# Kernel tuning notes

Measured on AMD Instinct MI355X. Metric: run time of the kernel, lower is better.

Reference implementation:

```python
import jax, jax.numpy as jnp
import numpy as np

NQ = 4  # n_qubits
NL = 2  # n_qlayers


def _rx(state, theta, wire):
    # state: (B, 2,...,2) complex; theta: (B,) RX rotation angles
    c = jnp.cos(theta * 0.5)[:, None]
    s = jnp.sin(theta * 0.5)[:, None]
    st = jnp.moveaxis(state, wire + 1, 1)
    sh = st.shape
    st = st.reshape(sh[0], 2, -1)
    a0, a1 = st[:, 0], st[:, 1]
    n0 = c * a0 - 1j * s * a1
    n1 = -1j * s * a0 + c * a1
    st = jnp.stack([n0, n1], axis=1).reshape(sh)
    return jnp.moveaxis(st, 1, wire + 1)


def _cnot(state, ctrl, tgt):
    st = jnp.moveaxis(state, (ctrl + 1, tgt + 1), (1, 2))
    st = jnp.stack([st[:, 0], st[:, 1, ::-1]], axis=1)
    return jnp.moveaxis(st, (1, 2), (ctrl + 1, tgt + 1))


def _vqc(y, W):
    # AngleEmbedding (RX) + BasicEntanglerLayers (RX + CNOT ring), PauliZ expvals.
    # y: (B, NQ) angles; W: (NL, NQ); returns (B, NQ)
    B = y.shape[0]
    state = jnp.zeros((B,) + (2,) * NQ, jnp.complex64)
    state = state.at[(slice(None),) + (0,) * NQ].set(1.0)
    for w in range(NQ):
        state = _rx(state, y[:, w], w)
    for l in range(W.shape[0]):
        for w in range(NQ):
            state = _rx(state, jnp.broadcast_to(W[l, w], (B,)), w)
        for w in range(NQ):
            state = _cnot(state, w, (w + 1) % NQ)
    probs = state.real ** 2 + state.imag ** 2  # (B, 2,2,2,2)
    z = jnp.array([1.0, -1.0], probs.dtype)
    exps = []
    for w in range(NQ):
        sign = z.reshape((1,) + (1,) * w + (2,) + (1,) * (NQ - 1 - w))
        exps.append(jnp.sum(probs * sign, axis=tuple(range(1, NQ + 1))))
    return jnp.stack(exps, axis=1)


def setup_inputs() -> dict:
    key = jax.random.key(0)
    ks = jax.random.split(key, 12)
    B, T, F, H = 1024, 64, 32, 8
    two_pi = 2.0 * np.pi
    return {
        "x": jax.random.normal(ks[0], (B, T, F), jnp.float32),
        "w_in": jax.random.normal(ks[1], (NQ, F + H), jnp.float32) * 0.1,
        "b_in": jnp.zeros((NQ,), jnp.float32),
        "w_out": jax.random.normal(ks[2], (H, NQ), jnp.float32) * 0.1,
        "b_out": jnp.zeros((H,), jnp.float32),
        "wq_f": jax.random.uniform(ks[3], (NL, NQ), jnp.float32, 0.0, two_pi),
        "wq_i": jax.random.uniform(ks[4], (NL, NQ), jnp.float32, 0.0, two_pi),
        "wq_u": jax.random.uniform(ks[5], (NL, NQ), jnp.float32, 0.0, two_pi),
        "wq_o": jax.random.uniform(ks[6], (NL, NQ), jnp.float32, 0.0, two_pi),
        "w_fc": jax.random.normal(ks[7], (1, H), jnp.float32) * 0.1,
        "b_fc": jnp.zeros((1,), jnp.float32),
    }


def reference(x, w_in, b_in, w_out, b_out, wq_f, wq_i, wq_u, wq_o, w_fc, b_fc):
    B, T, F = x.shape
    H = w_out.shape[0]
    h0 = jnp.zeros((B, H), x.dtype)
    c0 = jnp.zeros((B, H), x.dtype)

    def step(carry, x_t):
        h, c = carry
        v = jnp.concatenate([h, x_t], axis=1)           # (B, H+F)
        y = v @ w_in.T + b_in                           # (B, NQ)
        gate = lambda Wq: _vqc(y, Wq) @ w_out.T + b_out  # (B, H)
        f = jax.nn.sigmoid(gate(wq_f))
        i = jax.nn.sigmoid(gate(wq_i))
        g = jnp.tanh(gate(wq_u))
        o = jax.nn.sigmoid(gate(wq_o))
        c = f * c + i * g
        h = o * jnp.tanh(c)
        return (h, c), None

    (h, c), _ = jax.lax.scan(step, (h0, c0), jnp.swapaxes(x, 0, 1))
    return h @ w_fc.T + b_fc  # (B, 1)
```

## Files before the change

### kernel.cpp

```cpp
#include <hip/hip_runtime.h>
#include <math.h>


#define NQ 4
#define NL 2
#define BB 1024
#define TT 64
#define FF 32
#define HH 8

typedef float v2f __attribute__((ext_vector_type(2)));
typedef unsigned uv2 __attribute__((ext_vector_type(2)));
#define FMA2(a, b, c) __builtin_elementwise_fma((a), (b), (c))

#define RX_W(wv, cc, ss) do {                                   \
    const int str_ = 8 >> (wv);                                 \
    _Pragma("unroll")                                           \
    for (int lo_ = 0; lo_ < 16; ++lo_) {                        \
      if ((lo_ & str_) == 0) {                                  \
        const int hi_ = lo_ | str_;                             \
        float a0r = ar[lo_], a0i = ai[lo_];                     \
        float a1r = ar[hi_], a1i = ai[hi_];                     \
        ar[lo_] = fmaf((cc), a0r,  (ss)*a1i);                   \
        ai[lo_] = fmaf((cc), a0i, -(ss)*a1r);                   \
        ar[hi_] = fmaf((cc), a1r,  (ss)*a0i);                   \
        ai[hi_] = fmaf((cc), a1i, -(ss)*a0r);                   \
      }                                                         \
    }                                                           \
} while (0)

#define CNOT_W(cw, tw) do {                                     \
    const int cb_ = 1 << (3-(cw));                              \
    const int tb_ = 1 << (3-(tw));                              \
    _Pragma("unroll")                                           \
    for (int ix_ = 0; ix_ < 16; ++ix_) {                        \
      if ((ix_ & cb_) && !(ix_ & tb_)) {                        \
        const int jx_ = ix_ | tb_;                              \
        float tr_ = ar[ix_]; ar[ix_] = ar[jx_]; ar[jx_] = tr_;  \
        float ti_ = ai[ix_]; ai[ix_] = ai[jx_]; ai[jx_] = ti_;  \
      }                                                         \
    }                                                           \
} while (0)

#define QUAD_BCAST(x, CTRL) \
    __int_as_float(__builtin_amdgcn_mov_dpp(__float_as_int(x), (CTRL), 0xf, 0xf, true))
#define ROW_ROR(x, N) \
    __int_as_float(__builtin_amdgcn_mov_dpp(__float_as_int(x), 0x120 + (N), 0xf, 0xf, true))
#define SWZ_X16(x) \
    __int_as_float(__builtin_amdgcn_ds_swizzle(__float_as_int(x), 0x401F))

#if __has_builtin(__builtin_amdgcn_permlane16_swap)
__device__ __forceinline__ float permx16(float s, int lane) {
    uv2 r = __builtin_amdgcn_permlane16_swap(__builtin_bit_cast(unsigned, s),
                                             __builtin_bit_cast(unsigned, s),
                                             false, false);
    unsigned pick = (lane & 16) ? r.x : r.y;
    return __builtin_bit_cast(float, pick);
}
#else
__device__ __forceinline__ float permx16(float s, int lane) {
    (void)lane;
    return SWZ_X16(s);
}
#endif

#define TPASS(ST) do {                                                       \
    for (int i_ = threadIdx.x; i_ < 432; i_ += 64) {                         \
      int gw_ = i_ / 27; int r_ = i_ - gw_*27;                               \
      int hi_ = r_ / (ST); int lo_ = r_ - hi_*(ST);                          \
      float* row_ = sC + gw_*84; int p0_ = hi_*3*(ST) + lo_;                 \
      float f0_ = row_[p0_], f1_ = row_[p0_+(ST)], f2_ = row_[p0_+2*(ST)];   \
      row_[p0_]          = (f0_ + f1_ + f2_) * 0.3333333333333333f;          \
      row_[p0_+(ST)]     = (2.0f*f0_ - f1_ - f2_) * 0.3333333333333333f;     \
      row_[p0_+2*(ST)]   = (f1_ - f2_) * 0.5773502691896258f;                \
    }                                                                        \
    __syncthreads();                                                         \
} while (0)

#define C3V(k) ((k) == 26 ? c3t : (((k) & 1) ? cp[(k) >> 1].y : cp[(k) >> 1].x))

__global__ __launch_bounds__(64, 1)
void qlstm32p_kernel(const float* __restrict__ x,
                     const float* __restrict__ w_in,
                     const float* __restrict__ b_in,
                     const float* __restrict__ w_out,
                     const float* __restrict__ b_out,
                     const float* __restrict__ wq_f,
                     const float* __restrict__ wq_i,
                     const float* __restrict__ wq_u,
                     const float* __restrict__ wq_o,
                     const float* __restrict__ w_fc,
                     const float* __restrict__ b_fc,
                     float* __restrict__ out) {
    __shared__ float sC[16 * 84];
    __shared__ __align__(16) float sXW[2 * 65 * 4];

    const int lane = threadIdx.x;
    const int w    = lane & 3;
    const int j    = (lane >> 2) & 7;
    const int e    = lane >> 5;

    {
        const float b0 = b_in[0], b1 = b_in[1], b2 = b_in[2], b3 = b_in[3];
        #pragma unroll
        for (int r = 0; r < 8; ++r) {
            int slot = lane + 64 * r;
            int ee = slot >> 8;
            int tt = (slot >> 2) & 63;
            int ww = slot & 3;
            const float* xr = x + ((size_t)(blockIdx.x * 2 + ee) * TT + tt) * FF;
            float bb = (ww == 0) ? b0 : (ww == 1) ? b1 : (ww == 2) ? b2 : b3;
            const float* wrow = w_in + ww * 40 + 8;
            float acc = bb;
            #pragma unroll
            for (int k = 0; k < 8; ++k) {
                float4 xv = *reinterpret_cast<const float4*>(xr + 4 * k);
                acc = fmaf(xv.x, wrow[4*k+0],
                      fmaf(xv.y, wrow[4*k+1],
                      fmaf(xv.z, wrow[4*k+2],
                      fmaf(xv.w, wrow[4*k+3], acc))));
            }
            sXW[(ee * 65 + tt) * 4 + ww] = acc;
        }
    }

    for (int sidx = lane; sidx < 324; sidx += 64) {
        int g = sidx / 81;
        int p = sidx - g * 81;
        int t0 = p / 27; int rem = p - t0 * 27;
        int t1 = rem / 9; rem -= t1 * 9;
        int t2 = rem / 3; int t3 = rem - t2 * 3;

        const float s3h = 0.8660254037844386f;
        float c0 = (t0 == 0) ? 1.0f : 0.5f;
        float s0 = (t0 == 0) ? 0.0f : ((t0 == 1) ? s3h : -s3h);
        float c1 = (t1 == 0) ? 1.0f : 0.5f;
        float s1 = (t1 == 0) ? 0.0f : ((t1 == 1) ? s3h : -s3h);
        float c2 = (t2 == 0) ? 1.0f : 0.5f;
        float s2 = (t2 == 0) ? 0.0f : ((t2 == 1) ? s3h : -s3h);
        float c3v = (t3 == 0) ? 1.0f : 0.5f;
        float s3v = (t3 == 0) ? 0.0f : ((t3 == 1) ? s3h : -s3h);

        const float* wq = (g == 0) ? wq_f : (g == 1) ? wq_i : (g == 2) ? wq_u : wq_o;
        float lc[NL * NQ], ls[NL * NQ];
        #pragma unroll
        for (int a = 0; a < NL * NQ; ++a) {
            float ang = wq[a] * 0.5f;
            lc[a] = __cosf(ang);
            ls[a] = __sinf(ang);
        }

        float m01[4], m23[4];
        m01[0] = c0 * c1;  m01[1] = c0 * s1;  m01[2] = s0 * c1;  m01[3] = s0 * s1;
        m23[0] = c2 * c3v; m23[1] = c2 * s3v; m23[2] = s2 * c3v; m23[3] = s2 * s3v;
        float ar[16], ai[16];
        #pragma unroll
        for (int b0 = 0; b0 < 2; ++b0)
        #pragma unroll
        for (int b1 = 0; b1 < 2; ++b1)
        #pragma unroll
        for (int b2 = 0; b2 < 2; ++b2)
        #pragma unroll
        for (int b3 = 0; b3 < 2; ++b3) {
            const int idx = (b0 << 3) | (b1 << 2) | (b2 << 1) | b3;
            const int pc  = (b0 + b1 + b2 + b3) & 3;
            float m = m01[(b0 << 1) | b1] * m23[(b2 << 1) | b3];
            float re, im;
            if (pc == 0)      { re =  m;   im = 0.0f; }
            else if (pc == 1) { re = 0.0f; im = -m;   }
            else if (pc == 2) { re = -m;   im = 0.0f; }
            else              { re = 0.0f; im =  m;   }
            ar[idx] = re; ai[idx] = im;
        }

        #pragma unroll
        for (int l = 0; l < NL; ++l) {
            RX_W(0, lc[l*4+0], ls[l*4+0]);
            RX_W(1, lc[l*4+1], ls[l*4+1]);
            RX_W(2, lc[l*4+2], ls[l*4+2]);
            RX_W(3, lc[l*4+3], ls[l*4+3]);
            CNOT_W(0, 1); CNOT_W(1, 2); CNOT_W(2, 3); CNOT_W(3, 0);
        }

        float e0 = 0.f, e1 = 0.f, e2 = 0.f, e3 = 0.f;
        #pragma unroll
        for (int idx = 0; idx < 16; ++idx) {
            float pv = fmaf(ar[idx], ar[idx], ai[idx] * ai[idx]);
            e0 += (idx & 8) ? -pv : pv;
            e1 += (idx & 4) ? -pv : pv;
            e2 += (idx & 2) ? -pv : pv;
            e3 += (idx & 1) ? -pv : pv;
        }
        sC[(g * 4 + 0) * 84 + p] = e0;
        sC[(g * 4 + 1) * 84 + p] = e1;
        sC[(g * 4 + 2) * 84 + p] = e2;
        sC[(g * 4 + 3) * 84 + p] = e3;
    }
    __syncthreads();

    TPASS(27); TPASS(9); TPASS(3); TPASS(1);

    v2f E0[13], E1[13], E2[13];
    float e0s, e1s, e2s;
    {
        const float x0 = w_out[j * 4 + 0], x1 = w_out[j * 4 + 1];
        const float x2 = w_out[j * 4 + 2], x3 = w_out[j * 4 + 3];
        const float bo = b_out[j];
        const float* r0 = sC + (w * 4 + 0) * 84;
        const float* r1 = sC + (w * 4 + 1) * 84;
        const float* r2 = sC + (w * 4 + 2) * 84;
        const float* r3 = sC + (w * 4 + 3) * 84;
        #define DVAL(i) (fmaf(x0, r0[(i)], fmaf(x1, r1[(i)], fmaf(x2, r2[(i)], x3 * r3[(i)]))) \
                         + (((i) == 0) ? bo : 0.0f))
        #pragma unroll
        for (int p = 0; p < 13; ++p) {
            E0[p] = v2f{DVAL(6*p + 0), DVAL(6*p + 3)};
            E1[p] = v2f{DVAL(6*p + 1), DVAL(6*p + 4)};
            E2[p] = v2f{DVAL(6*p + 2), DVAL(6*p + 5)};
        }
        e0s = DVAL(78); e1s = DVAL(79); e2s = DVAL(80);
        #undef DVAL
    }
    #pragma unroll
    for (int i = 0; i < 13; ++i)
        asm volatile("" : "+v"(E0[i]), "+v"(E1[i]), "+v"(E2[i]));
    asm volatile("" : "+v"(e0s), "+v"(e1s), "+v"(e2s));

    const float wh  = w_in[w * 40 + j];
    const float wfc = w_fc[j];

    const bool  isG  = (w == 2);
    const float inS  = isG ? 2.0f : 1.0f;
    const float outS = isG ? 2.0f : 1.0f;
    const float outB = isG ? -1.0f : 0.0f;

    const float* sxw = sXW + e * 260 + w;

    float cc = 0.0f, hh = 0.0f;
    float xwv = sxw[0];

    for (int t = 0; t < TT; ++t) {
        float xwn = sxw[4 * (t + 1)];

        float p = hh * wh;
        float s = p + ROW_ROR(p, 4);
        s = s + ROW_ROR(s, 8);
        const float y = xwv + s + permx16(s, lane);

        const float u = __cosf(y), v = __sinf(y);
        const float u0 = QUAD_BCAST(u, 0x00), u1 = QUAD_BCAST(u, 0x55);
        const float u2 = QUAD_BCAST(u, 0xAA), u3 = QUAD_BCAST(u, 0xFF);
        const float v0 = QUAD_BCAST(v, 0x00), v1 = QUAD_BCAST(v, 0x55);
        const float v2 = QUAD_BCAST(v, 0xAA), v3 = QUAD_BCAST(v, 0xFF);

        const v2f u3p = {u3, u3}, v3p = {v3, v3};
        v2f cp[14];
        #pragma unroll
        for (int i = 0; i < 13; ++i)
            cp[i] = FMA2(u3p, E1[i], FMA2(v3p, E2[i], E0[i]));
        const float c3t = fmaf(u3, e1s, fmaf(v3, e2s, e0s));
        float c2v[9];
        #pragma unroll
        for (int i = 0; i < 9; ++i)
            c2v[i] = fmaf(u2, C3V(3*i + 1), fmaf(v2, C3V(3*i + 2), C3V(3*i)));
        const float c1a = fmaf(u1, c2v[1], fmaf(v1, c2v[2], c2v[0]));
        const float c1b = fmaf(u1, c2v[4], fmaf(v1, c2v[5], c2v[3]));
        const float c1c = fmaf(u1, c2v[7], fmaf(v1, c2v[8], c2v[6]));
        const float a = fmaf(u0, c1b, fmaf(v0, c1c, c1a));

        const float sg  = __builtin_amdgcn_rcpf(1.0f + __expf(-inS * a));
        const float act = fmaf(sg, outS, outB);

        const float fv = QUAD_BCAST(act, 0x00), iv = QUAD_BCAST(act, 0x55);
        const float gv = QUAD_BCAST(act, 0xAA), ov = QUAD_BCAST(act, 0xFF);

        cc = fmaf(fv, cc, iv * gv);
        const float th = fmaf(2.0f, __builtin_amdgcn_rcpf(1.0f + __expf(-2.0f * cc)), -1.0f);
        hh = ov * th;

        xwv = xwn;
    }

    float pf = hh * wfc;
    float sf = pf + ROW_ROR(pf, 4);
    sf = sf + ROW_ROR(sf, 8);
    sf = sf + permx16(sf, lane);
    if ((lane & 31) == 0) out[blockIdx.x * 2 + e] = sf + b_fc[0];
}

extern "C" void kernel_launch(void* const* d_in, const int* in_sizes, int n_in,
                              void* d_out, int out_size, void* d_ws, size_t ws_size,
                              hipStream_t stream) {
    const float* x     = (const float*)d_in[0];
    const float* w_in  = (const float*)d_in[1];
    const float* b_in  = (const float*)d_in[2];
    const float* w_out = (const float*)d_in[3];
    const float* b_out = (const float*)d_in[4];
    const float* wq_f  = (const float*)d_in[5];
    const float* wq_i  = (const float*)d_in[6];
    const float* wq_u  = (const float*)d_in[7];
    const float* wq_o  = (const float*)d_in[8];
    const float* w_fc  = (const float*)d_in[9];
    const float* b_fc  = (const float*)d_in[10];
    float* out = (float*)d_out;
    (void)in_sizes; (void)n_in; (void)out_size; (void)d_ws; (void)ws_size;

    qlstm32p_kernel<<<BB / 2, 64, 0, stream>>>(x, w_in, b_in, w_out, b_out,
                                               wq_f, wq_i, wq_u, wq_o,
                                               w_fc, b_fc, out);
}
```

Baseline: 105.0 us.

## Interleave two independent batch recurrences per wavefront to hide serial latency

Each wavefront now carries two batch elements' LSTM recurrences at once and interleaves their time steps, so the long dependent chain of one (shuffles, transcendentals, FMA tree) can overlap with the other. The grid halves to BB/4 blocks. The input projection is transposed in shared memory to a per-gate row layout with padded stride, read four timesteps at a time as float4, and uses two accumulators. The cost is more register pressure and half as many blocks, which on 256 CUs leaves fewer waves to hide latency.

```diff
diff --git a/kernel.cpp b/kernel.cpp
--- a/kernel.cpp
+++ b/kernel.cpp
@@ -79,21 +79,57 @@
 
 #define C3V(k) ((k) == 26 ? c3t : (((k) & 1) ? cp[(k) >> 1].y : cp[(k) >> 1].x))
 
+#define STEP(xwv, cc, hh) do {                                               \
+    float p_ = (hh) * wh;                                                    \
+    float s_ = p_ + ROW_ROR(p_, 4);                                          \
+    s_ = s_ + ROW_ROR(s_, 8);                                                \
+    const float y_ = (xwv) + s_ + permx16(s_, lane);                         \
+    const float u_ = __cosf(y_), vv_ = __sinf(y_);                           \
+    const float u0_ = QUAD_BCAST(u_, 0x00), u1_ = QUAD_BCAST(u_, 0x55);      \
+    const float u2_ = QUAD_BCAST(u_, 0xAA), u3_ = QUAD_BCAST(u_, 0xFF);      \
+    const float v0_ = QUAD_BCAST(vv_, 0x00), v1_ = QUAD_BCAST(vv_, 0x55);    \
+    const float v2_ = QUAD_BCAST(vv_, 0xAA), v3_ = QUAD_BCAST(vv_, 0xFF);    \
+    const v2f u3p_ = {u3_, u3_}, v3p_ = {v3_, v3_};                          \
+    v2f cp[14];                                                              \
+    _Pragma("unroll")                                                        \
+    for (int i_ = 0; i_ < 13; ++i_)                                          \
+        cp[i_] = FMA2(u3p_, E1[i_], FMA2(v3p_, E2[i_], E0[i_]));             \
+    const float c3t = fmaf(u3_, e1s, fmaf(v3_, e2s, e0s));                   \
+    float c2v[9];                                                            \
+    _Pragma("unroll")                                                        \
+    for (int i_ = 0; i_ < 9; ++i_)                                           \
+        c2v[i_] = fmaf(u2_, C3V(3*i_+1), fmaf(v2_, C3V(3*i_+2), C3V(3*i_))); \
+    const float c1a_ = fmaf(u1_, c2v[1], fmaf(v1_, c2v[2], c2v[0]));         \
+    const float c1b_ = fmaf(u1_, c2v[4], fmaf(v1_, c2v[5], c2v[3]));         \
+    const float c1c_ = fmaf(u1_, c2v[7], fmaf(v1_, c2v[8], c2v[6]));         \
+    const float a_ = fmaf(u0_, c1b_, fmaf(v0_, c1c_, c1a_));                 \
+    const float sg_ = __builtin_amdgcn_rcpf(1.0f + __expf(-inS * a_));       \
+    const float act_ = fmaf(sg_, outS, outB);                                \
+    const float fv_ = QUAD_BCAST(act_, 0x00), iv_ = QUAD_BCAST(act_, 0x55);  \
+    const float gv_ = QUAD_BCAST(act_, 0xAA), ov_ = QUAD_BCAST(act_, 0xFF);  \
+    (cc) = fmaf(fv_, (cc), iv_ * gv_);                                       \
+    const float th_ = fmaf(2.0f,                                             \
+        __builtin_amdgcn_rcpf(1.0f + __expf(-2.0f * (cc))), -1.0f);          \
+    (hh) = ov_ * th_;                                                        \
+} while (0)
+
+#define XSTRIDE 68
+
 __global__ __launch_bounds__(64, 1)
-void qlstm32p_kernel(const float* __restrict__ x,
-                     const float* __restrict__ w_in,
-                     const float* __restrict__ b_in,
-                     const float* __restrict__ w_out,
-                     const float* __restrict__ b_out,
-                     const float* __restrict__ wq_f,
-                     const float* __restrict__ wq_i,
-                     const float* __restrict__ wq_u,
-                     const float* __restrict__ wq_o,
-                     const float* __restrict__ w_fc,
-                     const float* __restrict__ b_fc,
-                     float* __restrict__ out) {
+void qlstm2x_kernel(const float* __restrict__ x,
+                    const float* __restrict__ w_in,
+                    const float* __restrict__ b_in,
+                    const float* __restrict__ w_out,
+                    const float* __restrict__ b_out,
+                    const float* __restrict__ wq_f,
+                    const float* __restrict__ wq_i,
+                    const float* __restrict__ wq_u,
+                    const float* __restrict__ wq_o,
+                    const float* __restrict__ w_fc,
+                    const float* __restrict__ b_fc,
+                    float* __restrict__ out) {
     __shared__ float sC[16 * 84];
-    __shared__ __align__(16) float sXW[2 * 65 * 4];
+    __shared__ __align__(16) float sXW[16 * XSTRIDE];
 
     const int lane = threadIdx.x;
     const int w    = lane & 3;
@@ -103,24 +139,29 @@
     {
         const float b0 = b_in[0], b1 = b_in[1], b2 = b_in[2], b3 = b_in[3];
         #pragma unroll
-        for (int r = 0; r < 8; ++r) {
+        for (int r = 0; r < 16; ++r) {
             int slot = lane + 64 * r;
             int ee = slot >> 8;
             int tt = (slot >> 2) & 63;
             int ww = slot & 3;
-            const float* xr = x + ((size_t)(blockIdx.x * 2 + ee) * TT + tt) * FF;
+            const float* xr = x + ((size_t)(blockIdx.x * 4 + ee) * TT + tt) * FF;
             float bb = (ww == 0) ? b0 : (ww == 1) ? b1 : (ww == 2) ? b2 : b3;
             const float* wrow = w_in + ww * 40 + 8;
-            float acc = bb;
+            float acc0 = bb, acc1 = 0.0f;
             #pragma unroll
-            for (int k = 0; k < 8; ++k) {
-                float4 xv = *reinterpret_cast<const float4*>(xr + 4 * k);
-                acc = fmaf(xv.x, wrow[4*k+0],
-                      fmaf(xv.y, wrow[4*k+1],
-                      fmaf(xv.z, wrow[4*k+2],
-                      fmaf(xv.w, wrow[4*k+3], acc))));
+            for (int k = 0; k < 8; k += 2) {
+                float4 xa = *reinterpret_cast<const float4*>(xr + 4 * k);
+                float4 xb = *reinterpret_cast<const float4*>(xr + 4 * k + 4);
+                acc0 = fmaf(xa.x, wrow[4*k+0],
+                       fmaf(xa.y, wrow[4*k+1],
+                       fmaf(xa.z, wrow[4*k+2],
+                       fmaf(xa.w, wrow[4*k+3], acc0))));
+                acc1 = fmaf(xb.x, wrow[4*k+4],
+                       fmaf(xb.y, wrow[4*k+5],
+                       fmaf(xb.z, wrow[4*k+6],
+                       fmaf(xb.w, wrow[4*k+7], acc1))));
             }
-            sXW[(ee * 65 + tt) * 4 + ww] = acc;
+            sXW[(ee * 4 + ww) * XSTRIDE + tt] = acc0 + acc1;
         }
     }
 
@@ -228,64 +269,45 @@
 
     const float wh  = w_in[w * 40 + j];
     const float wfc = w_fc[j];
-
     const bool  isG  = (w == 2);
     const float inS  = isG ? 2.0f : 1.0f;
     const float outS = isG ? 2.0f : 1.0f;
     const float outB = isG ? -1.0f : 0.0f;
 
-    const float* sxw = sXW + e * 260 + w;
-
-    float cc = 0.0f, hh = 0.0f;
-    float xwv = sxw[0];
-
-    for (int t = 0; t < TT; ++t) {
-        float xwn = sxw[4 * (t + 1)];
-
-        float p = hh * wh;
-        float s = p + ROW_ROR(p, 4);
-        s = s + ROW_ROR(s, 8);
-        const float y = xwv + s + permx16(s, lane);
-
-        const float u = __cosf(y), v = __sinf(y);
-        const float u0 = QUAD_BCAST(u, 0x00), u1 = QUAD_BCAST(u, 0x55);
-        const float u2 = QUAD_BCAST(u, 0xAA), u3 = QUAD_BCAST(u, 0xFF);
-        const float v0 = QUAD_BCAST(v, 0x00), v1 = QUAD_BCAST(v, 0x55);
-        const float v2 = QUAD_BCAST(v, 0xAA), v3 = QUAD_BCAST(v, 0xFF);
-
-        const v2f u3p = {u3, u3}, v3p = {v3, v3};
-        v2f cp[14];
-        #pragma unroll
-        for (int i = 0; i < 13; ++i)
-            cp[i] = FMA2(u3p, E1[i], FMA2(v3p, E2[i], E0[i]));
-        const float c3t = fmaf(u3, e1s, fmaf(v3, e2s, e0s));
-        float c2v[9];
-        #pragma unroll
-        for (int i = 0; i < 9; ++i)
-            c2v[i] = fmaf(u2, C3V(3*i + 1), fmaf(v2, C3V(3*i + 2), C3V(3*i)));
-        const float c1a = fmaf(u1, c2v[1], fmaf(v1, c2v[2], c2v[0]));
-        const float c1b = fmaf(u1, c2v[4], fmaf(v1, c2v[5], c2v[3]));
-        const float c1c = fmaf(u1, c2v[7], fmaf(v1, c2v[8], c2v[6]));
-        const float a = fmaf(u0, c1b, fmaf(v0, c1c, c1a));
-
-        const float sg  = __builtin_amdgcn_rcpf(1.0f + __expf(-inS * a));
-        const float act = fmaf(sg, outS, outB);
-
-        const float fv = QUAD_BCAST(act, 0x00), iv = QUAD_BCAST(act, 0x55);
-        const float gv = QUAD_BCAST(act, 0xAA), ov = QUAD_BCAST(act, 0xFF);
-
-        cc = fmaf(fv, cc, iv * gv);
-        const float th = fmaf(2.0f, __builtin_amdgcn_rcpf(1.0f + __expf(-2.0f * cc)), -1.0f);
-        hh = ov * th;
-
-        xwv = xwn;
-    }
-
-    float pf = hh * wfc;
-    float sf = pf + ROW_ROR(pf, 4);
-    sf = sf + ROW_ROR(sf, 8);
-    sf = sf + permx16(sf, lane);
-    if ((lane & 31) == 0) out[blockIdx.x * 2 + e] = sf + b_fc[0];
+    const float* pA = sXW + ((e * 2 + 0) * 4 + w) * XSTRIDE;
+    const float* pB = sXW + ((e * 2 + 1) * 4 + w) * XSTRIDE;
+
+    float ccA = 0.0f, hhA = 0.0f, ccB = 0.0f, hhB = 0.0f;
+    float4 xqA = *reinterpret_cast<const float4*>(pA);
+    float4 xqB = *reinterpret_cast<const float4*>(pB);
+
+    #pragma unroll 1
+    for (int g4 = 0; g4 < 16; ++g4) {
+        const int nx = (g4 < 15) ? (g4 + 1) * 4 : 60;
+        float4 xqAn = *reinterpret_cast<const float4*>(pA + nx);
+        float4 xqBn = *reinterpret_cast<const float4*>(pB + nx);
+
+        STEP(xqA.x, ccA, hhA); STEP(xqB.x, ccB, hhB);
+        STEP(xqA.y, ccA, hhA); STEP(xqB.y, ccB, hhB);
+        STEP(xqA.z, ccA, hhA); STEP(xqB.z, ccB, hhB);
+        STEP(xqA.w, ccA, hhA); STEP(xqB.w, ccB, hhB);
+
+        xqA = xqAn; xqB = xqBn;
+    }
+
+    float pfA = hhA * wfc;
+    float sfA = pfA + ROW_ROR(pfA, 4);
+    sfA = sfA + ROW_ROR(sfA, 8);
+    sfA = sfA + permx16(sfA, lane);
+    float pfB = hhB * wfc;
+    float sfB = pfB + ROW_ROR(pfB, 4);
+    sfB = sfB + ROW_ROR(sfB, 8);
+    sfB = sfB + permx16(sfB, lane);
+    if ((lane & 31) == 0) {
+        const int base = blockIdx.x * 4 + e * 2;
+        out[base]     = sfA + b_fc[0];
+        out[base + 1] = sfB + b_fc[0];
+    }
 }
 
 extern "C" void kernel_launch(void* const* d_in, const int* in_sizes, int n_in,
@@ -305,7 +327,7 @@
     float* out = (float*)d_out;
     (void)in_sizes; (void)n_in; (void)out_size; (void)d_ws; (void)ws_size;
 
-    qlstm32p_kernel<<<BB / 2, 64, 0, stream>>>(x, w_in, b_in, w_out, b_out,
-                                               wq_f, wq_i, wq_u, wq_o,
-                                               w_fc, b_fc, out);
+    qlstm2x_kernel<<<BB / 4, 64, 0, stream>>>(x, w_in, b_in, w_out, b_out,
+                                              wq_f, wq_i, wq_u, wq_o,
+                                              w_fc, b_fc, out);
 }
```

New measurement: 116.5 us. 1.11x slower.

## Replace tabulated 81-term VQC expansion with closed-form per-gate Heisenberg expectation

Applied to the files above, without the earlier changes.

Removes the per-block simulation of the 4-qubit circuit at 81 trig-basis points, the four shared-memory transform passes, and the 81-coefficient contraction in the recurrent loop. In their place it uses a closed-form expression for each gate's weighted PauliZ expectation, built from products of rotated cos/sin terms with a dozen precomputed constants. It also reorganises the x projection into per-wire contiguous rows so four timesteps load as one float4, unrolls the time loop by four, and splits the input dot product into two accumulators. The risk is that the derived closed form must match the circuit exactly for arbitrary weights.

```diff
diff --git a/kernel.cpp b/kernel.cpp
--- a/kernel.cpp
+++ b/kernel.cpp
@@ -9,38 +9,7 @@
 #define FF 32
 #define HH 8
 
-typedef float v2f __attribute__((ext_vector_type(2)));
 typedef unsigned uv2 __attribute__((ext_vector_type(2)));
-#define FMA2(a, b, c) __builtin_elementwise_fma((a), (b), (c))
-
-#define RX_W(wv, cc, ss) do {                                   \
-    const int str_ = 8 >> (wv);                                 \
-    _Pragma("unroll")                                           \
-    for (int lo_ = 0; lo_ < 16; ++lo_) {                        \
-      if ((lo_ & str_) == 0) {                                  \
-        const int hi_ = lo_ | str_;                             \
-        float a0r = ar[lo_], a0i = ai[lo_];                     \
-        float a1r = ar[hi_], a1i = ai[hi_];                     \
-        ar[lo_] = fmaf((cc), a0r,  (ss)*a1i);                   \
-        ai[lo_] = fmaf((cc), a0i, -(ss)*a1r);                   \
-        ar[hi_] = fmaf((cc), a1r,  (ss)*a0i);                   \
-        ai[hi_] = fmaf((cc), a1i, -(ss)*a0r);                   \
-      }                                                         \
-    }                                                           \
-} while (0)
-
-#define CNOT_W(cw, tw) do {                                     \
-    const int cb_ = 1 << (3-(cw));                              \
-    const int tb_ = 1 << (3-(tw));                              \
-    _Pragma("unroll")                                           \
-    for (int ix_ = 0; ix_ < 16; ++ix_) {                        \
-      if ((ix_ & cb_) && !(ix_ & tb_)) {                        \
-        const int jx_ = ix_ | tb_;                              \
-        float tr_ = ar[ix_]; ar[ix_] = ar[jx_]; ar[jx_] = tr_;  \
-        float ti_ = ai[ix_]; ai[ix_] = ai[jx_]; ai[jx_] = ti_;  \
-      }                                                         \
-    }                                                           \
-} while (0)
 
 #define QUAD_BCAST(x, CTRL) \
     __int_as_float(__builtin_amdgcn_mov_dpp(__float_as_int(x), (CTRL), 0xf, 0xf, true))
@@ -64,23 +33,10 @@
 }
 #endif
 
-#define TPASS(ST) do {                                                       \
-    for (int i_ = threadIdx.x; i_ < 432; i_ += 64) {                         \
-      int gw_ = i_ / 27; int r_ = i_ - gw_*27;                               \
-      int hi_ = r_ / (ST); int lo_ = r_ - hi_*(ST);                          \
-      float* row_ = sC + gw_*84; int p0_ = hi_*3*(ST) + lo_;                 \
-      float f0_ = row_[p0_], f1_ = row_[p0_+(ST)], f2_ = row_[p0_+2*(ST)];   \
-      row_[p0_]          = (f0_ + f1_ + f2_) * 0.3333333333333333f;          \
-      row_[p0_+(ST)]     = (2.0f*f0_ - f1_ - f2_) * 0.3333333333333333f;     \
-      row_[p0_+2*(ST)]   = (f1_ - f2_) * 0.5773502691896258f;                \
-    }                                                                        \
-    __syncthreads();                                                         \
-} while (0)
-
-#define C3V(k) ((k) == 26 ? c3t : (((k) & 1) ? cp[(k) >> 1].y : cp[(k) >> 1].x))
+#define XSTRIDE 68
 
 __global__ __launch_bounds__(64, 1)
-void qlstm32p_kernel(const float* __restrict__ x,
+void qlstm_hb_kernel(const float* __restrict__ x,
                      const float* __restrict__ w_in,
                      const float* __restrict__ b_in,
                      const float* __restrict__ w_out,
@@ -92,8 +48,7 @@
                      const float* __restrict__ w_fc,
                      const float* __restrict__ b_fc,
                      float* __restrict__ out) {
-    __shared__ float sC[16 * 84];
-    __shared__ __align__(16) float sXW[2 * 65 * 4];
+    __shared__ __align__(16) float sXW[8 * XSTRIDE];
 
     const int lane = threadIdx.x;
     const int w    = lane & 3;
@@ -111,175 +66,121 @@
             const float* xr = x + ((size_t)(blockIdx.x * 2 + ee) * TT + tt) * FF;
             float bb = (ww == 0) ? b0 : (ww == 1) ? b1 : (ww == 2) ? b2 : b3;
             const float* wrow = w_in + ww * 40 + 8;
-            float acc = bb;
+            float acc0 = bb, acc1 = 0.0f;
             #pragma unroll
-            for (int k = 0; k < 8; ++k) {
-                float4 xv = *reinterpret_cast<const float4*>(xr + 4 * k);
-                acc = fmaf(xv.x, wrow[4*k+0],
-                      fmaf(xv.y, wrow[4*k+1],
-                      fmaf(xv.z, wrow[4*k+2],
-                      fmaf(xv.w, wrow[4*k+3], acc))));
+            for (int k = 0; k < 8; k += 2) {
+                float4 xa = *reinterpret_cast<const float4*>(xr + 4 * k);
+                float4 xb = *reinterpret_cast<const float4*>(xr + 4 * k + 4);
+                acc0 = fmaf(xa.x, wrow[4*k+0],
+                       fmaf(xa.y, wrow[4*k+1],
+                       fmaf(xa.z, wrow[4*k+2],
+                       fmaf(xa.w, wrow[4*k+3], acc0))));
+                acc1 = fmaf(xb.x, wrow[4*k+4],
+                       fmaf(xb.y, wrow[4*k+5],
+                       fmaf(xb.z, wrow[4*k+6],
+                       fmaf(xb.w, wrow[4*k+7], acc1))));
             }
-            sXW[(ee * 65 + tt) * 4 + ww] = acc;
+            sXW[(ee * 4 + ww) * XSTRIDE + tt] = acc0 + acc1;
         }
     }
-
-    for (int sidx = lane; sidx < 324; sidx += 64) {
-        int g = sidx / 81;
-        int p = sidx - g * 81;
-        int t0 = p / 27; int rem = p - t0 * 27;
-        int t1 = rem / 9; rem -= t1 * 9;
-        int t2 = rem / 3; int t3 = rem - t2 * 3;
-
-        const float s3h = 0.8660254037844386f;
-        float c0 = (t0 == 0) ? 1.0f : 0.5f;
-        float s0 = (t0 == 0) ? 0.0f : ((t0 == 1) ? s3h : -s3h);
-        float c1 = (t1 == 0) ? 1.0f : 0.5f;
-        float s1 = (t1 == 0) ? 0.0f : ((t1 == 1) ? s3h : -s3h);
-        float c2 = (t2 == 0) ? 1.0f : 0.5f;
-        float s2 = (t2 == 0) ? 0.0f : ((t2 == 1) ? s3h : -s3h);
-        float c3v = (t3 == 0) ? 1.0f : 0.5f;
-        float s3v = (t3 == 0) ? 0.0f : ((t3 == 1) ? s3h : -s3h);
-
-        const float* wq = (g == 0) ? wq_f : (g == 1) ? wq_i : (g == 2) ? wq_u : wq_o;
-        float lc[NL * NQ], ls[NL * NQ];
-        #pragma unroll
-        for (int a = 0; a < NL * NQ; ++a) {
-            float ang = wq[a] * 0.5f;
-            lc[a] = __cosf(ang);
-            ls[a] = __sinf(ang);
-        }
-
-        float m01[4], m23[4];
-        m01[0] = c0 * c1;  m01[1] = c0 * s1;  m01[2] = s0 * c1;  m01[3] = s0 * s1;
-        m23[0] = c2 * c3v; m23[1] = c2 * s3v; m23[2] = s2 * c3v; m23[3] = s2 * s3v;
-        float ar[16], ai[16];
-        #pragma unroll
-        for (int b0 = 0; b0 < 2; ++b0)
-        #pragma unroll
-        for (int b1 = 0; b1 < 2; ++b1)
-        #pragma unroll
-        for (int b2 = 0; b2 < 2; ++b2)
-        #pragma unroll
-        for (int b3 = 0; b3 < 2; ++b3) {
-            const int idx = (b0 << 3) | (b1 << 2) | (b2 << 1) | b3;
-            const int pc  = (b0 + b1 + b2 + b3) & 3;
-            float m = m01[(b0 << 1) | b1] * m23[(b2 << 1) | b3];
-            float re, im;
-            if (pc == 0)      { re =  m;   im = 0.0f; }
-            else if (pc == 1) { re = 0.0f; im = -m;   }
-            else if (pc == 2) { re = -m;   im = 0.0f; }
-            else              { re = 0.0f; im =  m;   }
-            ar[idx] = re; ai[idx] = im;
-        }
-
-        #pragma unroll
-        for (int l = 0; l < NL; ++l) {
-            RX_W(0, lc[l*4+0], ls[l*4+0]);
-            RX_W(1, lc[l*4+1], ls[l*4+1]);
-            RX_W(2, lc[l*4+2], ls[l*4+2]);
-            RX_W(3, lc[l*4+3], ls[l*4+3]);
-            CNOT_W(0, 1); CNOT_W(1, 2); CNOT_W(2, 3); CNOT_W(3, 0);
-        }
-
-        float e0 = 0.f, e1 = 0.f, e2 = 0.f, e3 = 0.f;
-        #pragma unroll
-        for (int idx = 0; idx < 16; ++idx) {
-            float pv = fmaf(ar[idx], ar[idx], ai[idx] * ai[idx]);
-            e0 += (idx & 8) ? -pv : pv;
-            e1 += (idx & 4) ? -pv : pv;
-            e2 += (idx & 2) ? -pv : pv;
-            e3 += (idx & 1) ? -pv : pv;
-        }
-        sC[(g * 4 + 0) * 84 + p] = e0;
-        sC[(g * 4 + 1) * 84 + p] = e1;
-        sC[(g * 4 + 2) * 84 + p] = e2;
-        sC[(g * 4 + 3) * 84 + p] = e3;
-    }
     __syncthreads();
 
-    TPASS(27); TPASS(9); TPASS(3); TPASS(1);
-
-    v2f E0[13], E1[13], E2[13];
-    float e0s, e1s, e2s;
-    {
-        const float x0 = w_out[j * 4 + 0], x1 = w_out[j * 4 + 1];
-        const float x2 = w_out[j * 4 + 2], x3 = w_out[j * 4 + 3];
-        const float bo = b_out[j];
-        const float* r0 = sC + (w * 4 + 0) * 84;
-        const float* r1 = sC + (w * 4 + 1) * 84;
-        const float* r2 = sC + (w * 4 + 2) * 84;
-        const float* r3 = sC + (w * 4 + 3) * 84;
-        #define DVAL(i) (fmaf(x0, r0[(i)], fmaf(x1, r1[(i)], fmaf(x2, r2[(i)], x3 * r3[(i)]))) \
-                         + (((i) == 0) ? bo : 0.0f))
-        #pragma unroll
-        for (int p = 0; p < 13; ++p) {
-            E0[p] = v2f{DVAL(6*p + 0), DVAL(6*p + 3)};
-            E1[p] = v2f{DVAL(6*p + 1), DVAL(6*p + 4)};
-            E2[p] = v2f{DVAL(6*p + 2), DVAL(6*p + 5)};
-        }
-        e0s = DVAL(78); e1s = DVAL(79); e2s = DVAL(80);
-        #undef DVAL
-    }
-    #pragma unroll
-    for (int i = 0; i < 13; ++i)
-        asm volatile("" : "+v"(E0[i]), "+v"(E1[i]), "+v"(E2[i]));
-    asm volatile("" : "+v"(e0s), "+v"(e1s), "+v"(e2s));
+    const float* wq = (w == 0) ? wq_f : (w == 1) ? wq_i : (w == 2) ? wq_u : wq_o;
+    const float cph0 = __cosf(wq[0]), sph0 = __sinf(wq[0]);
+    const float cph1 = __cosf(wq[1]), sph1 = __sinf(wq[1]);
+    const float cph2 = __cosf(wq[2]), sph2 = __sinf(wq[2]);
+    const float cph3 = __cosf(wq[3]), sph3 = __sinf(wq[3]);
+    const float c0 = __cosf(wq[4]), s0 = __sinf(wq[4]);
+    const float c1 = __cosf(wq[5]), s1 = __sinf(wq[5]);
+    const float c2 = __cosf(wq[6]), s2 = __sinf(wq[6]);
+    const float c3 = __cosf(wq[7]), s3 = __sinf(wq[7]);
+    const float wo0 = w_out[j * 4 + 0], wo1 = w_out[j * 4 + 1];
+    const float wo2 = w_out[j * 4 + 2], wo3 = w_out[j * 4 + 3];
+    const float g0a = wo0 * (c1 * c2 * c3);
+    const float g0b = wo0 * (c1 * c2 * s3);
+    const float g0c = wo0 * (s1 * s2 * c3);
+    const float g0d = wo0 * (s1 * s2 * s3);
+    const float g1a = wo1 * (c0 * c1);
+    const float g1b = wo1 * (s0 * s1);
+    const float g2a = wo2 * (c0 * c1 * c2);
+    const float g2b = wo2 * (c0 * s1 * s2);
+    const float g3a = wo3 * (c0 * c1 * c2 * c3);
+    const float g3b = wo3 * (s0 * s1 * c2 * c3);
+    const float g3c = wo3 * (s0 * c1 * s2 * s3);
+    const float g3d = wo3 * (c0 * s1 * s2 * s3);
+    const float bo  = b_out[j];
 
     const float wh  = w_in[w * 40 + j];
     const float wfc = w_fc[j];
-
     const bool  isG  = (w == 2);
     const float inS  = isG ? 2.0f : 1.0f;
     const float outS = isG ? 2.0f : 1.0f;
     const float outB = isG ? -1.0f : 0.0f;
 
-    const float* sxw = sXW + e * 260 + w;
+    const float* sxw = sXW + (e * 4 + w) * XSTRIDE;
 
     float cc = 0.0f, hh = 0.0f;
-    float xwv = sxw[0];
-
-    for (int t = 0; t < TT; ++t) {
-        float xwn = sxw[4 * (t + 1)];
-
-        float p = hh * wh;
-        float s = p + ROW_ROR(p, 4);
-        s = s + ROW_ROR(s, 8);
-        const float y = xwv + s + permx16(s, lane);
-
-        const float u = __cosf(y), v = __sinf(y);
-        const float u0 = QUAD_BCAST(u, 0x00), u1 = QUAD_BCAST(u, 0x55);
-        const float u2 = QUAD_BCAST(u, 0xAA), u3 = QUAD_BCAST(u, 0xFF);
-        const float v0 = QUAD_BCAST(v, 0x00), v1 = QUAD_BCAST(v, 0x55);
-        const float v2 = QUAD_BCAST(v, 0xAA), v3 = QUAD_BCAST(v, 0xFF);
-
-        const v2f u3p = {u3, u3}, v3p = {v3, v3};
-        v2f cp[14];
-        #pragma unroll
-        for (int i = 0; i < 13; ++i)
-            cp[i] = FMA2(u3p, E1[i], FMA2(v3p, E2[i], E0[i]));
-        const float c3t = fmaf(u3, e1s, fmaf(v3, e2s, e0s));
-        float c2v[9];
-        #pragma unroll
-        for (int i = 0; i < 9; ++i)
-            c2v[i] = fmaf(u2, C3V(3*i + 1), fmaf(v2, C3V(3*i + 2), C3V(3*i)));
-        const float c1a = fmaf(u1, c2v[1], fmaf(v1, c2v[2], c2v[0]));
-        const float c1b = fmaf(u1, c2v[4], fmaf(v1, c2v[5], c2v[3]));
-        const float c1c = fmaf(u1, c2v[7], fmaf(v1, c2v[8], c2v[6]));
-        const float a = fmaf(u0, c1b, fmaf(v0, c1c, c1a));
-
-        const float sg  = __builtin_amdgcn_rcpf(1.0f + __expf(-inS * a));
-        const float act = fmaf(sg, outS, outB);
-
-        const float fv = QUAD_BCAST(act, 0x00), iv = QUAD_BCAST(act, 0x55);
-        const float gv = QUAD_BCAST(act, 0xAA), ov = QUAD_BCAST(act, 0xFF);
-
-        cc = fmaf(fv, cc, iv * gv);
-        const float th = fmaf(2.0f, __builtin_amdgcn_rcpf(1.0f + __expf(-2.0f * cc)), -1.0f);
-        hh = ov * th;
-
-        xwv = xwn;
+
+#define STEP(xwv) do {                                                        \
+          \
+    float p_ = hh * wh;                                                       \
+    float s_ = p_ + ROW_ROR(p_, 4);                                           \
+    s_ = s_ + ROW_ROR(s_, 8);                                                 \
+    const float y_ = (xwv) + s_ + permx16(s_, lane);                          \
+    const float u_ = __cosf(y_), v_ = __sinf(y_);                             \
+    const float u0_ = QUAD_BCAST(u_, 0x00), u1_ = QUAD_BCAST(u_, 0x55);       \
+    const float u2_ = QUAD_BCAST(u_, 0xAA), u3_ = QUAD_BCAST(u_, 0xFF);       \
+    const float v0_ = QUAD_BCAST(v_, 0x00), v1_ = QUAD_BCAST(v_, 0x55);       \
+    const float v2_ = QUAD_BCAST(v_, 0xAA), v3_ = QUAD_BCAST(v_, 0xFF);       \
+         \
+    const float t0_ = fmaf(cph0, u0_, -(sph0 * v0_));                         \
+    const float t1_ = fmaf(cph1, u1_, -(sph1 * v1_));                         \
+    const float t2_ = fmaf(cph2, u2_, -(sph2 * v2_));                         \
+    const float t3_ = fmaf(cph3, u3_, -(sph3 * v3_));                         \
+    const float r0_ = fmaf(sph0, u0_, cph0 * v0_);                            \
+    const float r1_ = fmaf(sph1, u1_, cph1 * v1_);                            \
+    const float r2_ = fmaf(sph2, u2_, cph2 * v2_);                            \
+    const float r3_ = fmaf(sph3, u3_, cph3 * v3_);                            \
+                                                           \
+    const float P_ = t1_ * t3_;                                               \
+    const float Q_ = r1_ * r3_;                                               \
+    const float S_ = t0_ * t2_;                                               \
+    const float T_ = r0_ * r2_;                                               \
+    const float U_ = t0_ * r2_;                                               \
+    const float V_ = r0_ * t2_;                                               \
+                                                  \
+    const float mP_ = fmaf(g0a, t0_, fmaf(g0d, r0_, g2a));                    \
+    const float mQ_ = fmaf(g0c, t0_, fmaf(g0b, r0_, g2b));                    \
+    float a_ = fmaf(mP_, P_, fmaf(mQ_, Q_, bo));                              \
+    const float e1_ = fmaf(g1a, S_, g1b * T_);                                \
+    a_ = fmaf(e1_, t3_, a_);                                                  \
+    a_ = fmaf(g3a, S_, a_);                                                   \
+    a_ = fmaf(g3b, T_, a_);                                                   \
+    a_ = fmaf(g3c, U_, a_);                                                   \
+    a_ = fmaf(g3d, V_, a_);                                                   \
+                     \
+    const float sg_ = __builtin_amdgcn_rcpf(1.0f + __expf(-inS * a_));        \
+    const float act_ = fmaf(sg_, outS, outB);                                 \
+    const float fv_ = QUAD_BCAST(act_, 0x00), iv_ = QUAD_BCAST(act_, 0x55);   \
+    const float gv_ = QUAD_BCAST(act_, 0xAA), ov_ = QUAD_BCAST(act_, 0xFF);   \
+    cc = fmaf(fv_, cc, iv_ * gv_);                                            \
+    const float th_ = fmaf(2.0f,                                              \
+        __builtin_amdgcn_rcpf(1.0f + __expf(-2.0f * cc)), -1.0f);             \
+    hh = ov_ * th_;                                                           \
+} while (0)
+
+    float4 xq = *reinterpret_cast<const float4*>(sxw);
+    #pragma unroll 1
+    for (int g4 = 0; g4 < 16; ++g4) {
+        const int nx = (g4 < 15) ? (g4 + 1) * 4 : 60;
+        float4 xqn = *reinterpret_cast<const float4*>(sxw + nx);
+        STEP(xq.x);
+        STEP(xq.y);
+        STEP(xq.z);
+        STEP(xq.w);
+        xq = xqn;
     }
+#undef STEP
 
     float pf = hh * wfc;
     float sf = pf + ROW_ROR(pf, 4);
@@ -305,7 +206,7 @@
     float* out = (float*)d_out;
     (void)in_sizes; (void)n_in; (void)out_size; (void)d_ws; (void)ws_size;
 
-    qlstm32p_kernel<<<BB / 2, 64, 0, stream>>>(x, w_in, b_in, w_out, b_out,
+    qlstm_hb_kernel<<<BB / 2, 64, 0, stream>>>(x, w_in, b_in, w_out, b_out,
                                                wq_f, wq_i, wq_u, wq_o,
                                                w_fc, b_fc, out);
 }
```

Result: faster. 88.96 us (-15.3%).
